# Performance work log

Measured on AMD Instinct MI355X. Metric: run time of the kernel, lower is better.

## Reference

```python
import jax, jax.numpy as jnp
import numpy as np

N_NODES = 100000
N_EDGES = 1600000
NUM_RELS = 200
NUM_BASES = 4
IN_FEAT = 20   # hardcoded by `view(-1, 1, 20)` in the torch source
OUT_FEAT = 20
SUBMAT_IN = IN_FEAT // NUM_BASES   # 5
SUBMAT_OUT = OUT_FEAT // NUM_BASES # 5


def setup_inputs() -> dict:
    key = jax.random.key(0)
    ks = jax.random.split(key, 9)
    return {
        "h": jax.random.normal(ks[0], (N_NODES, IN_FEAT), dtype=jnp.float32),
        "weight": jax.random.normal(ks[1], (NUM_RELS, NUM_BASES * SUBMAT_IN * SUBMAT_OUT), dtype=jnp.float32),
        "bias_term": jax.random.normal(ks[2], (NUM_RELS, OUT_FEAT), dtype=jnp.float32),
        "gate_weight": jax.random.normal(ks[3], (NUM_RELS, OUT_FEAT, 1), dtype=jnp.float32),
        "gate_bias": jax.random.normal(ks[4], (NUM_RELS, 1), dtype=jnp.float32),
        "loop_weight": jax.random.normal(ks[5], (IN_FEAT, OUT_FEAT), dtype=jnp.float32),
        "edge_src": jax.random.randint(ks[6], (N_EDGES,), 0, N_NODES, dtype=jnp.int32),
        "edge_dst": jax.random.randint(ks[7], (N_EDGES,), 0, N_NODES, dtype=jnp.int32),
        "etype": jax.random.randint(ks[8], (NUM_RELS,), 0, NUM_RELS, dtype=jnp.int32) if False else jax.random.randint(ks[8], (N_EDGES,), 0, NUM_RELS, dtype=jnp.int32),
    }


def reference(h, weight, bias_term, gate_weight, gate_bias, loop_weight, edge_src, edge_dst, etype):
    n_nodes = h.shape[0]
    # self-loop message (dropout=0.0 -> identity)
    loop_message = h @ loop_weight                                    # [N, out]
    # per-edge relation-indexed gathers
    W = weight[etype].reshape(-1, NUM_BASES, SUBMAT_IN, SUBMAT_OUT)   # [E, B, si, so]
    src = h[edge_src]                                                 # [E, in]
    node = src.reshape(-1, NUM_BASES, SUBMAT_IN)                      # [E, B, si]
    # block-diagonal small matmul
    msg = jnp.einsum('ebi,ebio->ebo', node, W).reshape(-1, OUT_FEAT)  # [E, out]
    # gate: sigmoid(<full src node, gate_weight_r> + gate_bias_r)
    gw = gate_weight[etype, :, 0]                                     # [E, out(=20=in)]
    gb = gate_bias[etype, 0]                                          # [E]
    gate = jax.nn.sigmoid(jnp.sum(src * gw, axis=-1) + gb)            # [E]
    msg = gate[:, None] * (msg + bias_term[etype])                    # [E, out]
    # scatter-sum aggregation to destination nodes (zero init for isolated nodes)
    agg = jax.ops.segment_sum(msg, edge_dst, num_segments=n_nodes)    # [N, out]
    return jax.nn.relu(agg + loop_message)
```

## Files before the change

### kernel.cpp

```cpp
#include <hip/hip_runtime.h>
#include <hip/hip_fp16.h>
#include <math.h>

#define IN_FEAT 20
#define OUT_FEAT 20
#define NUM_BASES 4
#define SUBMAT_IN 5
#define SUBMAT_OUT 5
#define NUM_RELS 200
#define CAP 64
#define NPB 160
#define BCAP 3072

__global__ void zero_kernel(int* __restrict__ p, int n) {
    int i = blockIdx.x * blockDim.x + threadIdx.x;
    if (i < n) p[i] = 0;
}

__global__ void __launch_bounds__(1024)
bucket_scatter_kernel(const int* __restrict__ edge_src,
                      const int* __restrict__ edge_dst,
                      const int* __restrict__ etype,
                      int* __restrict__ cursor,
                      int2* __restrict__ bucketed,
                      int n_edges, int nb) {
    __shared__ int lhist[1024];
    __shared__ int lbase[1024];
    __shared__ int lrank[1024];
    int tid = threadIdx.x;
    for (int i = tid; i < nb; i += 1024) { lhist[i] = 0; lrank[i] = 0; }
    __syncthreads();

    int e0 = blockIdx.x * 4096 + tid * 4;
    int s[4], d[4], t[4], bk[4];
    bool val[4];
    if (e0 + 3 < n_edges) {
        int4 sv = *(const int4*)(edge_src + e0);
        int4 dv = *(const int4*)(edge_dst + e0);
        int4 tv = *(const int4*)(etype + e0);
        s[0]=sv.x; s[1]=sv.y; s[2]=sv.z; s[3]=sv.w;
        d[0]=dv.x; d[1]=dv.y; d[2]=dv.z; d[3]=dv.w;
        t[0]=tv.x; t[1]=tv.y; t[2]=tv.z; t[3]=tv.w;
        val[0]=val[1]=val[2]=val[3]=true;
    } else {
#pragma unroll
        for (int k = 0; k < 4; ++k) {
            int e = e0 + k;
            val[k] = (e < n_edges);
            s[k] = val[k] ? edge_src[e] : 0;
            d[k] = val[k] ? edge_dst[e] : 0;
            t[k] = val[k] ? etype[e] : 0;
        }
    }
#pragma unroll
    for (int k = 0; k < 4; ++k) {
        bk[k] = d[k] / NPB;
        if (val[k]) atomicAdd(&lhist[bk[k]], 1);
    }
    __syncthreads();
    for (int i = tid; i < nb; i += 1024)
        if (lhist[i] > 0) lbase[i] = atomicAdd(&cursor[i], lhist[i]);
    __syncthreads();
#pragma unroll
    for (int k = 0; k < 4; ++k) {
        if (val[k]) {
            int r = atomicAdd(&lrank[bk[k]], 1);
            int off = lbase[bk[k]] + r;
            if (off < BCAP) {
                unsigned packed = (unsigned)s[k] | ((unsigned)t[k] << 17);
                bucketed[(size_t)bk[k] * BCAP + off] = make_int2(d[k], (int)packed);
            }
        }
    }
}

__global__ void __launch_bounds__(1024)
bucket_place_kernel(const int* __restrict__ cursor,
                    const int2* __restrict__ bucketed,
                    unsigned* __restrict__ records,
                    int* __restrict__ cnt,
                    int n_nodes) {
    __shared__ unsigned img[NPB * CAP];
    __shared__ int lcnt[NPB];
    int b = blockIdx.x, tid = threadIdx.x;
    int node0 = b * NPB;
    for (int i = tid; i < NPB; i += 1024) lcnt[i] = 0;
    __syncthreads();
    int m = cursor[b]; if (m > BCAP) m = BCAP;
    for (int i = tid; i < m; i += 1024) {
        int2 r = bucketed[(size_t)b * BCAP + i];
        int dl = r.x - node0;
        int sl = atomicAdd(&lcnt[dl], 1);
        if (sl < CAP) img[dl * CAP + sl] = (unsigned)r.y;
    }
    __syncthreads();
    for (int i = tid; i < NPB; i += 1024) {
        int v = node0 + i;
        if (v < n_nodes) cnt[v] = lcnt[i];
    }
    const int W4 = NPB * CAP / 4;
    uint4* g4 = (uint4*)records + (size_t)node0 * (CAP / 4);
    const uint4* l4 = (const uint4*)img;
    for (int i = tid; i < W4; i += 1024) {
        int v = node0 + (i / (CAP / 4));
        if (v < n_nodes) g4[i] = l4[i];
    }
}

__global__ void __launch_bounds__(1024, 4)
gather_kernel(const float* __restrict__ h,
              const float* __restrict__ loop_weight,
              const float* __restrict__ weight,
              const float* __restrict__ bias_term,
              const float* __restrict__ gate_weight,
              const float* __restrict__ gate_bias,
              const int* __restrict__ cnt,
              const unsigned* __restrict__ records,
              float* __restrict__ out, int n_nodes, int n_groups) {
    __shared__ __half lds_wt[100 * NUM_RELS];
    __shared__ float  lds_gwt[IN_FEAT * NUM_RELS];
    __shared__ float  lds_gb[NUM_RELS];
    __shared__ float  lds_lw[IN_FEAT * OUT_FEAT];
    int tid = threadIdx.x;
    for (int idx = tid; idx < 100 * NUM_RELS; idx += 1024) {
        int t = idx / 100, j = idx % 100;
        lds_wt[j * NUM_RELS + t] = __float2half(weight[idx]);
    }
    for (int idx = tid; idx < IN_FEAT * NUM_RELS; idx += 1024) {
        int t = idx / IN_FEAT, i = idx % IN_FEAT;
        lds_gwt[i * NUM_RELS + t] = gate_weight[idx];
    }
    for (int idx = tid; idx < NUM_RELS; idx += 1024) lds_gb[idx] = gate_bias[idx];
    for (int idx = tid; idx < IN_FEAT * OUT_FEAT; idx += 1024) lds_lw[idx] = loop_weight[idx];
    __syncthreads();

    int wave = blockIdx.x * 16 + (tid >> 6);
    int nwaves = gridDim.x * 16;
    int l = tid & 63;
    int l16 = l & 15;

    for (int grp = wave; grp < n_groups; grp += nwaves) {
        int v = grp * 4 + (l >> 4);
        bool valid = (v < n_nodes);
        int c = valid ? cnt[v] : 0;
        if (c > CAP) c = CAP;

        float acc[OUT_FEAT];
#pragma unroll
        for (int j = 0; j < OUT_FEAT; ++j) acc[j] = 0.0f;

        if (valid) {
#pragma unroll
            for (int i0 = 0; i0 < 2; ++i0) {
                int i = l16 + i0 * 16;
                if (i < IN_FEAT) {
                    float s = h[(size_t)v * IN_FEAT + i];
#pragma unroll
                    for (int j = 0; j < OUT_FEAT; ++j)
                        acc[j] = fmaf(s, lds_lw[i * OUT_FEAT + j], acc[j]);
                }
            }
        }

#pragma unroll
        for (int it = 0; it < 4; ++it) {
            int slot = l16 + it * 16;
            if (valid && slot < c) {
                unsigned p = records[(size_t)v * CAP + slot];
                int srcid = (int)(p & 0x1FFFFu);
                int t = (int)(p >> 17);

                float src[IN_FEAT];
                const float4* hp = (const float4*)(h + (size_t)srcid * IN_FEAT);
#pragma unroll
                for (int i = 0; i < IN_FEAT / 4; ++i) {
                    float4 tv = hp[i];
                    src[4 * i + 0] = tv.x; src[4 * i + 1] = tv.y;
                    src[4 * i + 2] = tv.z; src[4 * i + 3] = tv.w;
                }

                float g = lds_gb[t];
#pragma unroll
                for (int i = 0; i < IN_FEAT; ++i)
                    g = fmaf(src[i], lds_gwt[i * NUM_RELS + t], g);
                g = 1.0f / (1.0f + __expf(-g));

                const __half* wt = lds_wt + t;
#pragma unroll
                for (int b = 0; b < NUM_BASES; ++b) {
#pragma unroll
                    for (int i = 0; i < SUBMAT_IN; ++i) {
                        float sv = g * src[b * SUBMAT_IN + i];
#pragma unroll
                        for (int o = 0; o < SUBMAT_OUT; ++o) {
                            float w = __half2float(wt[(size_t)(b * 25 + i * 5 + o) * NUM_RELS]);
                            acc[b * SUBMAT_OUT + o] = fmaf(sv, w, acc[b * SUBMAT_OUT + o]);
                        }
                    }
                }
                const float4* btp = (const float4*)(bias_term + (size_t)t * OUT_FEAT);
#pragma unroll
                for (int k = 0; k < OUT_FEAT / 4; ++k) {
                    float4 bv = btp[k];
                    acc[4 * k + 0] = fmaf(g, bv.x, acc[4 * k + 0]);
                    acc[4 * k + 1] = fmaf(g, bv.y, acc[4 * k + 1]);
                    acc[4 * k + 2] = fmaf(g, bv.z, acc[4 * k + 2]);
                    acc[4 * k + 3] = fmaf(g, bv.w, acc[4 * k + 3]);
                }
            }
        }

#pragma unroll
        for (int mask = 8; mask > 0; mask >>= 1) {
#pragma unroll
            for (int j = 0; j < OUT_FEAT; ++j)
                acc[j] += __shfl_xor(acc[j], mask, 16);
        }

        if (valid && l16 < OUT_FEAT / 4) {
            float4 tv;
            tv.x = fmaxf(acc[4 * l16 + 0], 0.0f);
            tv.y = fmaxf(acc[4 * l16 + 1], 0.0f);
            tv.z = fmaxf(acc[4 * l16 + 2], 0.0f);
            tv.w = fmaxf(acc[4 * l16 + 3], 0.0f);
            ((float4*)(out + (size_t)v * OUT_FEAT))[l16] = tv;
        }
    }
}

__global__ void loop_msg_kernel(const float* __restrict__ h,
                                const float* __restrict__ loop_weight,
                                float* __restrict__ out, int n_nodes) {
    int v = blockIdx.x * blockDim.x + threadIdx.x;
    if (v >= n_nodes) return;
    float src[IN_FEAT];
    const float4* hp = (const float4*)(h + (size_t)v * IN_FEAT);
#pragma unroll
    for (int i = 0; i < IN_FEAT / 4; ++i) {
        float4 t = hp[i];
        src[4 * i + 0] = t.x; src[4 * i + 1] = t.y;
        src[4 * i + 2] = t.z; src[4 * i + 3] = t.w;
    }
    float acc[OUT_FEAT];
#pragma unroll
    for (int j = 0; j < OUT_FEAT; ++j) acc[j] = 0.0f;
#pragma unroll
    for (int i = 0; i < IN_FEAT; ++i) {
        float s = src[i];
#pragma unroll
        for (int j = 0; j < OUT_FEAT; ++j)
            acc[j] = fmaf(s, loop_weight[i * OUT_FEAT + j], acc[j]);
    }
    float4* op = (float4*)(out + (size_t)v * OUT_FEAT);
#pragma unroll
    for (int j = 0; j < OUT_FEAT / 4; ++j) {
        float4 t;
        t.x = acc[4 * j + 0]; t.y = acc[4 * j + 1];
        t.z = acc[4 * j + 2]; t.w = acc[4 * j + 3];
        op[j] = t;
    }
}

__global__ void edge_atomic_kernel(const float* __restrict__ h,
                                   const float* __restrict__ weight,
                                   const float* __restrict__ bias_term,
                                   const float* __restrict__ gate_weight,
                                   const float* __restrict__ gate_bias,
                                   const int* __restrict__ edge_src,
                                   const int* __restrict__ edge_dst,
                                   const int* __restrict__ etype,
                                   float* __restrict__ out, int n_edges) {
    int e = blockIdx.x * blockDim.x + threadIdx.x;
    if (e >= n_edges) return;
    int s = edge_src[e], d = edge_dst[e], t = etype[e];
    float src[IN_FEAT];
    const float4* hp = (const float4*)(h + (size_t)s * IN_FEAT);
#pragma unroll
    for (int i = 0; i < IN_FEAT / 4; ++i) {
        float4 v = hp[i];
        src[4 * i + 0] = v.x; src[4 * i + 1] = v.y;
        src[4 * i + 2] = v.z; src[4 * i + 3] = v.w;
    }
    const float* W = weight + (size_t)t * 100;
    float msg[OUT_FEAT];
#pragma unroll
    for (int j = 0; j < OUT_FEAT; ++j) msg[j] = 0.0f;
#pragma unroll
    for (int b = 0; b < NUM_BASES; ++b)
#pragma unroll
        for (int i = 0; i < SUBMAT_IN; ++i) {
            float sv = src[b * SUBMAT_IN + i];
#pragma unroll
            for (int o = 0; o < SUBMAT_OUT; ++o)
                msg[b * SUBMAT_OUT + o] =
                    fmaf(sv, W[(b * SUBMAT_IN + i) * SUBMAT_OUT + o],
                         msg[b * SUBMAT_OUT + o]);
        }
    const float* gw = gate_weight + (size_t)t * OUT_FEAT;
    float g = gate_bias[t];
#pragma unroll
    for (int i = 0; i < IN_FEAT; ++i) g = fmaf(src[i], gw[i], g);
    g = 1.0f / (1.0f + __expf(-g));
    const float* bt = bias_term + (size_t)t * OUT_FEAT;
    float* dstp = out + (size_t)d * OUT_FEAT;
#pragma unroll
    for (int j = 0; j < OUT_FEAT; ++j) atomicAdd(&dstp[j], g * (msg[j] + bt[j]));
}

__global__ void relu_kernel(float* __restrict__ out, int n4) {
    int i = blockIdx.x * blockDim.x + threadIdx.x;
    if (i >= n4) return;
    float4* p = (float4*)out;
    float4 v = p[i];
    v.x = fmaxf(v.x, 0.0f); v.y = fmaxf(v.y, 0.0f);
    v.z = fmaxf(v.z, 0.0f); v.w = fmaxf(v.w, 0.0f);
    p[i] = v;
}

extern "C" void kernel_launch(void* const* d_in, const int* in_sizes, int n_in,
                              void* d_out, int out_size, void* d_ws, size_t ws_size,
                              hipStream_t stream) {
    const float* h           = (const float*)d_in[0];
    const float* weight      = (const float*)d_in[1];
    const float* bias_term   = (const float*)d_in[2];
    const float* gate_weight = (const float*)d_in[3];
    const float* gate_bias   = (const float*)d_in[4];
    const float* loop_weight = (const float*)d_in[5];
    const int* edge_src      = (const int*)d_in[6];
    const int* edge_dst      = (const int*)d_in[7];
    const int* etype         = (const int*)d_in[8];
    float* out = (float*)d_out;

    const int n_nodes = in_sizes[0] / IN_FEAT;
    const int n_edges = in_sizes[6];
    const int nb = (n_nodes + NPB - 1) / NPB;

    size_t off_cursor   = 0;
    size_t off_bucketed = (((size_t)nb * 4 + 127) / 128) * 128;
    size_t off_records  = ((off_bucketed + (size_t)nb * BCAP * 8 + 127) / 128) * 128;
    size_t off_cnt      = ((off_records + (size_t)n_nodes * CAP * 4 + 127) / 128) * 128;
    size_t need = off_cnt + (size_t)n_nodes * 4;

    bool ok = (ws_size >= need) && (n_nodes <= (1 << 17)) && (nb <= 1024) &&
              (in_sizes[4] == NUM_RELS) && (in_sizes[1] == NUM_RELS * 100) &&
              (in_sizes[5] == IN_FEAT * OUT_FEAT);

    if (ok) {
        int*  cursor   = (int*)((char*)d_ws + off_cursor);
        int2* bucketed = (int2*)((char*)d_ws + off_bucketed);
        unsigned* records = (unsigned*)((char*)d_ws + off_records);
        int*  cnt      = (int*)((char*)d_ws + off_cnt);

        zero_kernel<<<(nb + 255) / 256, 256, 0, stream>>>(cursor, nb);
        bucket_scatter_kernel<<<(n_edges + 4095) / 4096, 1024, 0, stream>>>(
            edge_src, edge_dst, etype, cursor, bucketed, n_edges, nb);
        bucket_place_kernel<<<nb, 1024, 0, stream>>>(
            cursor, bucketed, records, cnt, n_nodes);
        int n_groups = (n_nodes + 3) / 4;
        gather_kernel<<<512, 1024, 0, stream>>>(
            h, loop_weight, weight, bias_term, gate_weight, gate_bias,
            cnt, records, out, n_nodes, n_groups);
    } else {
        loop_msg_kernel<<<(n_nodes + 255) / 256, 256, 0, stream>>>(
            h, loop_weight, out, n_nodes);
        edge_atomic_kernel<<<(n_edges + 255) / 256, 256, 0, stream>>>(
            h, weight, bias_term, gate_weight, gate_bias,
            edge_src, edge_dst, etype, out, n_edges);
        relu_kernel<<<(n_nodes * OUT_FEAT / 4 + 255) / 256, 256, 0, stream>>>(
            out, n_nodes * OUT_FEAT / 4);
    }
}
```

Measured before the change: 205.4 us.

## Repack relation weights per-relation as half2 in LDS, cache bias_term in LDS

Changes the LDS layout of relation weights from relation-strided halves to contiguous per-relation half2 pairs (padded row of 51), so each lane reads its relation's weights as packed pairs instead of 100 strided 16-bit loads. Bias_term is now staged in LDS with a stride of 21 rather than read from global memory per edge. The zero kernel is replaced with hipMemsetAsync. Lanes in a wave work on different relations, so the new per-relation contiguous layout may cause LDS bank conflicts, and the larger dynamic LDS footprint may lower occupancy.

```diff
diff --git a/kernel.cpp b/kernel.cpp
--- a/kernel.cpp
+++ b/kernel.cpp
@@ -12,10 +12,12 @@
 #define NPB 160
 #define BCAP 3072
 
-__global__ void zero_kernel(int* __restrict__ p, int n) {
-    int i = blockIdx.x * blockDim.x + threadIdx.x;
-    if (i < n) p[i] = 0;
-}
+#define LW_OFF   0
+#define GB_OFF   (LW_OFF + 400)
+#define GWT_OFF  (GB_OFF + 200)
+#define BT_OFF   (GWT_OFF + 4000)
+#define W2_OFF   (BT_OFF + 4200)
+#define LDS_DWORDS (W2_OFF + 10200)
 
 __global__ void __launch_bounds__(1024)
 bucket_scatter_kernel(const int* __restrict__ edge_src,
@@ -117,21 +119,31 @@
               const int* __restrict__ cnt,
               const unsigned* __restrict__ records,
               float* __restrict__ out, int n_nodes, int n_groups) {
-    __shared__ __half lds_wt[100 * NUM_RELS];
-    __shared__ float  lds_gwt[IN_FEAT * NUM_RELS];
-    __shared__ float  lds_gb[NUM_RELS];
-    __shared__ float  lds_lw[IN_FEAT * OUT_FEAT];
+    extern __shared__ float smem[];
+    float*   lds_lw  = smem + LW_OFF;
+    float*   lds_gb  = smem + GB_OFF;
+    float*   lds_gwt = smem + GWT_OFF;
+    float*   lds_bt  = smem + BT_OFF;
+    __half2* lds_w2  = (__half2*)(smem + W2_OFF);
+
     int tid = threadIdx.x;
-    for (int idx = tid; idx < 100 * NUM_RELS; idx += 1024) {
-        int t = idx / 100, j = idx % 100;
-        lds_wt[j * NUM_RELS + t] = __float2half(weight[idx]);
-    }
+    for (int idx = tid; idx < IN_FEAT * OUT_FEAT; idx += 1024) lds_lw[idx] = loop_weight[idx];
+    for (int idx = tid; idx < NUM_RELS; idx += 1024) lds_gb[idx] = gate_bias[idx];
     for (int idx = tid; idx < IN_FEAT * NUM_RELS; idx += 1024) {
         int t = idx / IN_FEAT, i = idx % IN_FEAT;
         lds_gwt[i * NUM_RELS + t] = gate_weight[idx];
     }
-    for (int idx = tid; idx < NUM_RELS; idx += 1024) lds_gb[idx] = gate_bias[idx];
-    for (int idx = tid; idx < IN_FEAT * OUT_FEAT; idx += 1024) lds_lw[idx] = loop_weight[idx];
+    for (int idx = tid; idx < NUM_RELS * OUT_FEAT; idx += 1024) {
+        int t = idx / OUT_FEAT, o = idx % OUT_FEAT;
+        lds_bt[t * 21 + o] = bias_term[idx];
+    }
+    for (int idx = tid; idx < NUM_RELS * 51; idx += 1024) {
+        int t = idx / 51, j2 = idx % 51;
+        int j = 2 * j2;
+        float lo = (j < 100) ? weight[t * 100 + j] : 0.0f;
+        float hi = (j + 1 < 100) ? weight[t * 100 + j + 1] : 0.0f;
+        lds_w2[t * 51 + j2] = __floats2half2_rn(lo, hi);
+    }
     __syncthreads();
 
     int wave = blockIdx.x * 16 + (tid >> 6);
@@ -185,7 +197,7 @@
                     g = fmaf(src[i], lds_gwt[i * NUM_RELS + t], g);
                 g = 1.0f / (1.0f + __expf(-g));
 
-                const __half* wt = lds_wt + t;
+                const __half2* w2 = lds_w2 + t * 51;
 #pragma unroll
                 for (int b = 0; b < NUM_BASES; ++b) {
 #pragma unroll
@@ -193,20 +205,17 @@
                         float sv = g * src[b * SUBMAT_IN + i];
 #pragma unroll
                         for (int o = 0; o < SUBMAT_OUT; ++o) {
-                            float w = __half2float(wt[(size_t)(b * 25 + i * 5 + o) * NUM_RELS]);
+                            const int j = b * 25 + i * 5 + o;
+                            __half2 pr = w2[j >> 1];
+                            float w = (j & 1) ? __high2float(pr) : __low2float(pr);
                             acc[b * SUBMAT_OUT + o] = fmaf(sv, w, acc[b * SUBMAT_OUT + o]);
                         }
                     }
                 }
-                const float4* btp = (const float4*)(bias_term + (size_t)t * OUT_FEAT);
-#pragma unroll
-                for (int k = 0; k < OUT_FEAT / 4; ++k) {
-                    float4 bv = btp[k];
-                    acc[4 * k + 0] = fmaf(g, bv.x, acc[4 * k + 0]);
-                    acc[4 * k + 1] = fmaf(g, bv.y, acc[4 * k + 1]);
-                    acc[4 * k + 2] = fmaf(g, bv.z, acc[4 * k + 2]);
-                    acc[4 * k + 3] = fmaf(g, bv.w, acc[4 * k + 3]);
-                }
+                const float* bt = lds_bt + t * 21;
+#pragma unroll
+                for (int o = 0; o < OUT_FEAT; ++o)
+                    acc[o] = fmaf(g, bt[o], acc[o]);
             }
         }
 
@@ -351,13 +360,13 @@
         unsigned* records = (unsigned*)((char*)d_ws + off_records);
         int*  cnt      = (int*)((char*)d_ws + off_cnt);
 
-        zero_kernel<<<(nb + 255) / 256, 256, 0, stream>>>(cursor, nb);
+        hipMemsetAsync(cursor, 0, (size_t)nb * 4, stream);
         bucket_scatter_kernel<<<(n_edges + 4095) / 4096, 1024, 0, stream>>>(
             edge_src, edge_dst, etype, cursor, bucketed, n_edges, nb);
         bucket_place_kernel<<<nb, 1024, 0, stream>>>(
             cursor, bucketed, records, cnt, n_nodes);
         int n_groups = (n_nodes + 3) / 4;
-        gather_kernel<<<512, 1024, 0, stream>>>(
+        gather_kernel<<<512, 1024, LDS_DWORDS * 4, stream>>>(
             h, loop_weight, weight, bias_term, gate_weight, gate_bias,
             cnt, records, out, n_nodes, n_groups);
     } else {
```

After: 214.9 us. 4.6% more time.

## Gather half-precision source features and repack relation weights in LDS

Applied to the files above, without the earlier changes.

Adds a pre-pass that converts node features to padded fp16 rows (48 bytes), so each edge's random source gather moves less data. In the gather kernel, the relation weights are stored row-major as half2 pairs and read with 128-bit LDS loads, and bias_term and gate weights are also cached in LDS with vectorized reads. The gate is applied to the source vector once, up front. The zero kernel is replaced by a memset. This costs an extra conversion kernel and adds fp16 rounding of source features, which may cost accuracy. LDS use grows to about 76 KB, which may reduce occupancy.

```diff
diff --git a/kernel.cpp b/kernel.cpp
--- a/kernel.cpp
+++ b/kernel.cpp
@@ -11,10 +11,34 @@
 #define CAP 64
 #define NPB 160
 #define BCAP 3072
-
-__global__ void zero_kernel(int* __restrict__ p, int n) {
-    int i = blockIdx.x * blockDim.x + threadIdx.x;
-    if (i < n) p[i] = 0;
+#define H16_STRIDE 24
+
+#define LW_OFF   0
+#define GB_OFF   400
+#define GW_OFF   600
+#define BT_OFF   4600
+#define W2_OFF   8600
+#define LDS_DWORDS 19000
+
+__global__ void h2half_kernel(const float* __restrict__ h,
+                              __half* __restrict__ h16, int n_nodes) {
+    int v = blockIdx.x * blockDim.x + threadIdx.x;
+    if (v >= n_nodes) return;
+    const float4* hp = (const float4*)(h + (size_t)v * IN_FEAT);
+    __half hb[H16_STRIDE];
+#pragma unroll
+    for (int i = 0; i < IN_FEAT / 4; ++i) {
+        float4 t = hp[i];
+        hb[4 * i + 0] = __float2half(t.x);
+        hb[4 * i + 1] = __float2half(t.y);
+        hb[4 * i + 2] = __float2half(t.z);
+        hb[4 * i + 3] = __float2half(t.w);
+    }
+#pragma unroll
+    for (int i = IN_FEAT; i < H16_STRIDE; ++i) hb[i] = __half(0.0f);
+    uint4* dst = (uint4*)(h16 + (size_t)v * H16_STRIDE);
+#pragma unroll
+    for (int k = 0; k < 3; ++k) dst[k] = ((const uint4*)hb)[k];
 }
 
 __global__ void __launch_bounds__(1024)
@@ -109,6 +133,7 @@
 
 __global__ void __launch_bounds__(1024, 4)
 gather_kernel(const float* __restrict__ h,
+              const __half* __restrict__ h16,
               const float* __restrict__ loop_weight,
               const float* __restrict__ weight,
               const float* __restrict__ bias_term,
@@ -117,21 +142,25 @@
               const int* __restrict__ cnt,
               const unsigned* __restrict__ records,
               float* __restrict__ out, int n_nodes, int n_groups) {
-    __shared__ __half lds_wt[100 * NUM_RELS];
-    __shared__ float  lds_gwt[IN_FEAT * NUM_RELS];
-    __shared__ float  lds_gb[NUM_RELS];
-    __shared__ float  lds_lw[IN_FEAT * OUT_FEAT];
+    extern __shared__ float smem[];
     int tid = threadIdx.x;
-    for (int idx = tid; idx < 100 * NUM_RELS; idx += 1024) {
-        int t = idx / 100, j = idx % 100;
-        lds_wt[j * NUM_RELS + t] = __float2half(weight[idx]);
-    }
-    for (int idx = tid; idx < IN_FEAT * NUM_RELS; idx += 1024) {
-        int t = idx / IN_FEAT, i = idx % IN_FEAT;
-        lds_gwt[i * NUM_RELS + t] = gate_weight[idx];
-    }
-    for (int idx = tid; idx < NUM_RELS; idx += 1024) lds_gb[idx] = gate_bias[idx];
-    for (int idx = tid; idx < IN_FEAT * OUT_FEAT; idx += 1024) lds_lw[idx] = loop_weight[idx];
+
+    for (int idx = tid; idx < IN_FEAT * OUT_FEAT; idx += 1024)
+        smem[LW_OFF + idx] = loop_weight[idx];
+    for (int idx = tid; idx < NUM_RELS; idx += 1024)
+        smem[GB_OFF + idx] = gate_bias[idx];
+    for (int idx = tid; idx < NUM_RELS * IN_FEAT; idx += 1024)
+        smem[GW_OFF + idx] = gate_weight[idx];
+    for (int idx = tid; idx < NUM_RELS * OUT_FEAT; idx += 1024)
+        smem[BT_OFF + idx] = bias_term[idx];
+    for (int idx = tid; idx < NUM_RELS * 52; idx += 1024) {
+        int t = idx / 52, j2 = idx % 52;
+        int j = 2 * j2;
+        float lo = (j < 100) ? weight[t * 100 + j] : 0.0f;
+        float hi = (j + 1 < 100) ? weight[t * 100 + j + 1] : 0.0f;
+        __half2 pr = __floats2half2_rn(lo, hi);
+        smem[W2_OFF + idx] = *(float*)&pr;
+    }
     __syncthreads();
 
     int wave = blockIdx.x * 16 + (tid >> 6);
@@ -155,9 +184,15 @@
                 int i = l16 + i0 * 16;
                 if (i < IN_FEAT) {
                     float s = h[(size_t)v * IN_FEAT + i];
-#pragma unroll
-                    for (int j = 0; j < OUT_FEAT; ++j)
-                        acc[j] = fmaf(s, lds_lw[i * OUT_FEAT + j], acc[j]);
+                    const float4* lwr = (const float4*)(smem + LW_OFF) + i * 5;
+#pragma unroll
+                    for (int k = 0; k < 5; ++k) {
+                        float4 wv = lwr[k];
+                        acc[4 * k + 0] = fmaf(s, wv.x, acc[4 * k + 0]);
+                        acc[4 * k + 1] = fmaf(s, wv.y, acc[4 * k + 1]);
+                        acc[4 * k + 2] = fmaf(s, wv.z, acc[4 * k + 2]);
+                        acc[4 * k + 3] = fmaf(s, wv.w, acc[4 * k + 3]);
+                    }
                 }
             }
         }
@@ -170,38 +205,67 @@
                 int srcid = (int)(p & 0x1FFFFu);
                 int t = (int)(p >> 17);
 
+                const uint4* hp = (const uint4*)(h16 + (size_t)srcid * H16_STRIDE);
+                uint4 ha = hp[0], hbq = hp[1], hc = hp[2];
                 float src[IN_FEAT];
-                const float4* hp = (const float4*)(h + (size_t)srcid * IN_FEAT);
-#pragma unroll
-                for (int i = 0; i < IN_FEAT / 4; ++i) {
-                    float4 tv = hp[i];
-                    src[4 * i + 0] = tv.x; src[4 * i + 1] = tv.y;
-                    src[4 * i + 2] = tv.z; src[4 * i + 3] = tv.w;
+                {
+                    const unsigned dw[6] = {ha.x, ha.y, ha.z, ha.w, hbq.x, hbq.y};
+#pragma unroll
+                    for (int k = 0; k < 6; ++k) {
+                        float2 f = __half22float2(*(const __half2*)&dw[k]);
+                        src[2 * k + 0] = f.x; src[2 * k + 1] = f.y;
+                    }
+                    const unsigned dw2[4] = {hbq.z, hbq.w, hc.x, hc.y};
+#pragma unroll
+                    for (int k = 0; k < 4; ++k) {
+                        float2 f = __half22float2(*(const __half2*)&dw2[k]);
+                        src[12 + 2 * k + 0] = f.x; src[12 + 2 * k + 1] = f.y;
+                    }
                 }
 
-                float g = lds_gb[t];
-#pragma unroll
-                for (int i = 0; i < IN_FEAT; ++i)
-                    g = fmaf(src[i], lds_gwt[i * NUM_RELS + t], g);
+                float g = smem[GB_OFF + t];
+                const float4* gwr = (const float4*)(smem + GW_OFF) + t * 5;
+#pragma unroll
+                for (int k = 0; k < 5; ++k) {
+                    float4 wv = gwr[k];
+                    g = fmaf(src[4 * k + 0], wv.x, g);
+                    g = fmaf(src[4 * k + 1], wv.y, g);
+                    g = fmaf(src[4 * k + 2], wv.z, g);
+                    g = fmaf(src[4 * k + 3], wv.w, g);
+                }
                 g = 1.0f / (1.0f + __expf(-g));
 
-                const __half* wt = lds_wt + t;
-#pragma unroll
-                for (int b = 0; b < NUM_BASES; ++b) {
-#pragma unroll
-                    for (int i = 0; i < SUBMAT_IN; ++i) {
-                        float sv = g * src[b * SUBMAT_IN + i];
-#pragma unroll
-                        for (int o = 0; o < SUBMAT_OUT; ++o) {
-                            float w = __half2float(wt[(size_t)(b * 25 + i * 5 + o) * NUM_RELS]);
-                            acc[b * SUBMAT_OUT + o] = fmaf(sv, w, acc[b * SUBMAT_OUT + o]);
+#pragma unroll
+                for (int i = 0; i < IN_FEAT; ++i) src[i] *= g;
+
+                const uint4* wq4 = (const uint4*)(smem + W2_OFF) + (size_t)t * 13;
+#pragma unroll
+                for (int q = 0; q < 13; ++q) {
+                    uint4 wq = wq4[q];
+                    float wv[8];
+                    {
+                        float2 f0 = __half22float2(*(const __half2*)&wq.x);
+                        float2 f1 = __half22float2(*(const __half2*)&wq.y);
+                        float2 f2 = __half22float2(*(const __half2*)&wq.z);
+                        float2 f3 = __half22float2(*(const __half2*)&wq.w);
+                        wv[0]=f0.x; wv[1]=f0.y; wv[2]=f1.x; wv[3]=f1.y;
+                        wv[4]=f2.x; wv[5]=f2.y; wv[6]=f3.x; wv[7]=f3.y;
+                    }
+#pragma unroll
+                    for (int r = 0; r < 8; ++r) {
+                        const int j = q * 8 + r;
+                        if (j < 100) {
+                            const int b = j / 25, io = j % 25;
+                            const int i = io / 5, o = io % 5;
+                            acc[b * 5 + o] = fmaf(src[b * 5 + i], wv[r], acc[b * 5 + o]);
                         }
                     }
                 }
-                const float4* btp = (const float4*)(bias_term + (size_t)t * OUT_FEAT);
-#pragma unroll
-                for (int k = 0; k < OUT_FEAT / 4; ++k) {
-                    float4 bv = btp[k];
+
+                const float4* btr = (const float4*)(smem + BT_OFF) + t * 5;
+#pragma unroll
+                for (int k = 0; k < 5; ++k) {
+                    float4 bv = btr[k];
                     acc[4 * k + 0] = fmaf(g, bv.x, acc[4 * k + 0]);
                     acc[4 * k + 1] = fmaf(g, bv.y, acc[4 * k + 1]);
                     acc[4 * k + 2] = fmaf(g, bv.z, acc[4 * k + 2]);
@@ -339,7 +403,8 @@
     size_t off_bucketed = (((size_t)nb * 4 + 127) / 128) * 128;
     size_t off_records  = ((off_bucketed + (size_t)nb * BCAP * 8 + 127) / 128) * 128;
     size_t off_cnt      = ((off_records + (size_t)n_nodes * CAP * 4 + 127) / 128) * 128;
-    size_t need = off_cnt + (size_t)n_nodes * 4;
+    size_t off_h16      = ((off_cnt + (size_t)n_nodes * 4 + 127) / 128) * 128;
+    size_t need = off_h16 + (size_t)n_nodes * H16_STRIDE * 2;
 
     bool ok = (ws_size >= need) && (n_nodes <= (1 << 17)) && (nb <= 1024) &&
               (in_sizes[4] == NUM_RELS) && (in_sizes[1] == NUM_RELS * 100) &&
@@ -350,15 +415,17 @@
         int2* bucketed = (int2*)((char*)d_ws + off_bucketed);
         unsigned* records = (unsigned*)((char*)d_ws + off_records);
         int*  cnt      = (int*)((char*)d_ws + off_cnt);
-
-        zero_kernel<<<(nb + 255) / 256, 256, 0, stream>>>(cursor, nb);
+        __half* h16    = (__half*)((char*)d_ws + off_h16);
+
+        hipMemsetAsync(cursor, 0, (size_t)nb * 4, stream);
+        h2half_kernel<<<(n_nodes + 255) / 256, 256, 0, stream>>>(h, h16, n_nodes);
         bucket_scatter_kernel<<<(n_edges + 4095) / 4096, 1024, 0, stream>>>(
             edge_src, edge_dst, etype, cursor, bucketed, n_edges, nb);
         bucket_place_kernel<<<nb, 1024, 0, stream>>>(
             cursor, bucketed, records, cnt, n_nodes);
         int n_groups = (n_nodes + 3) / 4;
-        gather_kernel<<<512, 1024, 0, stream>>>(
-            h, loop_weight, weight, bias_term, gate_weight, gate_bias,
+        gather_kernel<<<512, 1024, LDS_DWORDS * 4, stream>>>(
+            h, h16, loop_weight, weight, bias_term, gate_weight, gate_bias,
             cnt, records, out, n_nodes, n_groups);
     } else {
         loop_msg_kernel<<<(n_nodes + 255) / 256, 256, 0, stream>>>(
```

Result: slower. 225.0 us (+9.6%).
